# Kernel tuning notes

Measured on AMD Instinct MI355X. Metric: run time of the kernel, lower is better.

## Reference

```python
import jax, jax.numpy as jnp
import numpy as np

B, N, D, H = 2, 2048, 1024, 16
HD = D // H
SCALE = HD ** -0.5


def setup_inputs() -> dict:
    key = jax.random.key(0)
    ks = jax.random.split(key, 9)
    s = D ** -0.5
    return {
        "x": jax.random.normal(ks[0], (B, N, D), dtype=jnp.float32),
        "Wq": jax.random.normal(ks[1], (D, D), dtype=jnp.float32) * s,
        "bq": jax.random.normal(ks[2], (D,), dtype=jnp.float32) * 0.01,
        "Wk": jax.random.normal(ks[3], (D, D), dtype=jnp.float32) * s,
        "bk": jax.random.normal(ks[4], (D,), dtype=jnp.float32) * 0.01,
        "Wv": jax.random.normal(ks[5], (D, D), dtype=jnp.float32) * s,
        "bv": jax.random.normal(ks[6], (D,), dtype=jnp.float32) * 0.01,
        "Wo": jax.random.normal(ks[7], (D, D), dtype=jnp.float32) * s,
        "bo": jax.random.normal(ks[8], (D,), dtype=jnp.float32) * 0.01,
    }


def reference(x, Wq, bq, Wk, bk, Wv, bv, Wo, bo):
    # Q/K/V projections (torch Linear: x @ W.T + b), split into heads: (B,H,N,HD)
    def proj(W, b):
        return (x @ W.T + b).reshape(B, N, H, HD).transpose(0, 2, 1, 3)

    q = proj(Wq, bq)
    k = proj(Wk, bk)
    v = proj(Wv, bv)
    # Scaled dot-product attention with explicit (B,H,N,N) scores
    scores = jnp.einsum("bhnd,bhmd->bhnm", q, k) * SCALE
    attn = jax.nn.softmax(scores, axis=-1)
    y = jnp.einsum("bhnm,bhmd->bhnd", attn, v)
    y = y.transpose(0, 2, 1, 3).reshape(B, N, D)
    # Output projection
    return y @ Wo.T + bo
```

## Files before the change

kernel.cpp:

```cpp
#include <hip/hip_runtime.h>

#define BB 2
#define NN 2048
#define DD 1024
#define HH 16
#define HD 64
#define SCALE 0.125f

typedef unsigned short u16;
typedef unsigned int u32;
typedef __attribute__((ext_vector_type(2))) unsigned int u32x2;
typedef __attribute__((ext_vector_type(4))) short short4v;
typedef __attribute__((ext_vector_type(8))) short short8;
typedef __attribute__((ext_vector_type(4))) float float4v;
typedef __attribute__((ext_vector_type(16))) float f32x16;

__device__ __forceinline__ float b2f(u16 u) {
    union { float f; u32 i; } x; x.i = ((u32)u) << 16; return x.f;
}
__device__ __forceinline__ u16 f2b(float f) {
    union { float f; u32 i; } x; x.f = f;
    u32 i = x.i;
    return (u16)((i + 0x7fffu + ((i >> 16) & 1u)) >> 16);
}

#if __has_builtin(__builtin_amdgcn_exp2f)
#define EXP2F(x) __builtin_amdgcn_exp2f(x)
#else
#define EXP2F(x) __expf((x) * 0.69314718055994531f)
#endif

#if __has_builtin(__builtin_amdgcn_rcpf)
#define RCPF(x) __builtin_amdgcn_rcpf(x)
#else
#define RCPF(x) (1.0f / (x))
#endif

#if __has_builtin(__builtin_amdgcn_permlane32_swap)
#define PSWAP(a, b, ra, rb)                                                  \
    { u32x2 _r = __builtin_amdgcn_permlane32_swap((a), (b), false, false);   \
      (ra) = _r[0]; (rb) = _r[1]; }
#else
#define PSWAP(a, b, ra, rb)                                                  \
    { u32 _xa = (u32)__shfl_xor((int)(a), 32, 64);                           \
      u32 _xb = (u32)__shfl_xor((int)(b), 32, 64);                           \
      (ra) = hi ? _xb : (a); (rb) = hi ? (b) : _xa; }
#endif

__device__ __forceinline__ u32 cvtpk(float a, float b) {
    u32 r;
    asm("v_cvt_pk_bf16_f32 %0, %1, %2" : "=v"(r) : "v"(a), "v"(b));
    return r;
}

__device__ __forceinline__ void gl_lds16(const u16* g, u16* l) {
    __builtin_amdgcn_global_load_lds(
        (__attribute__((address_space(1))) void*)(void*)g,
        (__attribute__((address_space(3))) void*)l, 16, 0, 0);
}

__global__ __launch_bounds__(256) void cvt_all(
    const float* __restrict__ x,
    const float* __restrict__ Wq, const float* __restrict__ Wk,
    const float* __restrict__ Wv, const float* __restrict__ Wo,
    u16* __restrict__ xb, u16* __restrict__ W4)
{
    int e = (blockIdx.x * 256 + threadIdx.x) * 8;
    const float* s;
    u16* d;
    if (e < 4194304) { s = x + e; d = xb + e; }
    else {
        int e2 = e - 4194304;
        int which = e2 >> 20;
        int off = e2 & 1048575;
        s = ((which == 0) ? Wq : (which == 1) ? Wk : (which == 2) ? Wv : Wo) + off;
        d = W4 + e2;
    }
    float4v a = *(const float4v*)s;
    float4v b = *(const float4v*)(s + 4);
    short8 r;
    r[0] = (short)f2b(a[0]); r[1] = (short)f2b(a[1]);
    r[2] = (short)f2b(a[2]); r[3] = (short)f2b(a[3]);
    r[4] = (short)f2b(b[0]); r[5] = (short)f2b(b[1]);
    r[6] = (short)f2b(b[2]); r[7] = (short)f2b(b[3]);
    *(short8*)d = r;
}

__global__ __launch_bounds__(512) void gemm_qkv(
    const u16* __restrict__ xb,
    const u16* __restrict__ Wqb, const float* __restrict__ bq,
    const u16* __restrict__ Wkb, const float* __restrict__ bk,
    const u16* __restrict__ Wvb, const float* __restrict__ bv,
    u16* __restrict__ Qo, u16* __restrict__ Ko, u16* __restrict__ Vt)
{
    const int lid = blockIdx.y * 12 + blockIdx.x;
    const int seq = (lid & 7) * 24 + (lid >> 3);
    const int tm = seq / 12;
    const int tn = seq % 12;
    const int mat = tn >> 2;
    const int tnq = tn & 3;

    const u16* __restrict__ W     = (mat == 0) ? Wqb : (mat == 1) ? Wkb : Wvb;
    const float* __restrict__ bias = (mat == 0) ? bq : (mat == 1) ? bk : bv;

    __shared__ u16 As[4][256 * 32];
    __shared__ u16 Bs[4][256 * 32];

    const int tid  = threadIdx.x;
    const int wave = tid >> 6, lane = tid & 63;
    const int wm = wave >> 2, wn = wave & 3;
    const int quad = lane >> 4, l16 = lane & 15;

    const int sr = tid >> 2, sc = tid & 3;
    const u16* ga0 = &xb[(size_t)(tm * 256 + sr) * DD + sc * 8];
    const u16* ga1 = ga0 + (size_t)128 * DD;
    const u16* gb0 = &W [(size_t)(tnq * 256 + sr) * DD + sc * 8];
    const u16* gb1 = gb0 + (size_t)128 * DD;

    float4v acc[8][4] = {};

    #pragma unroll
    for (int s = 0; s < 3; ++s) {
        const int ks = s << 5;
        gl_lds16(ga0 + ks, &As[s][tid * 8]);
        gl_lds16(ga1 + ks, &As[s][(512 + tid) * 8]);
        gl_lds16(gb0 + ks, &Bs[s][tid * 8]);
        gl_lds16(gb1 + ks, &Bs[s][(512 + tid) * 8]);
    }

    for (int it = 0; it < 32; ++it) {
        asm volatile("s_waitcnt vmcnt(8)" ::: "memory");
        __builtin_amdgcn_s_barrier();

        const int k3 = ((it + 3) & 31) << 5;
        const int b3 = (it + 3) & 3;
        gl_lds16(ga0 + k3, &As[b3][tid * 8]);
        gl_lds16(ga1 + k3, &As[b3][(512 + tid) * 8]);
        gl_lds16(gb0 + k3, &Bs[b3][tid * 8]);
        gl_lds16(gb1 + k3, &Bs[b3][(512 + tid) * 8]);

        const int cb = it & 3;
        short8 af[8], bf[4];
        #pragma unroll
        for (int mi = 0; mi < 8; ++mi)
            af[mi] = *(const short8*)&As[cb][(wm * 128 + mi * 16 + l16) * 32 + quad * 8];
        #pragma unroll
        for (int ni = 0; ni < 4; ++ni)
            bf[ni] = *(const short8*)&Bs[cb][(wn * 64 + ni * 16 + l16) * 32 + quad * 8];

        #pragma unroll
        for (int mi = 0; mi < 8; ++mi)
            #pragma unroll
            for (int ni = 0; ni < 4; ++ni)
                acc[mi][ni] = __builtin_amdgcn_mfma_f32_16x16x32_bf16(
                    af[mi], bf[ni], acc[mi][ni], 0, 0, 0);
    }
    asm volatile("s_waitcnt vmcnt(0)" ::: "memory");

    #pragma unroll
    for (int mi = 0; mi < 8; ++mi) {
        #pragma unroll
        for (int ni = 0; ni < 4; ++ni) {
            int cc = tnq * 256 + wn * 64 + ni * 16 + l16;
            int h = cc >> 6, hd = cc & 63;
            float bv_ = bias[cc];
            if (mat == 2) {
                short4v v4;
                #pragma unroll
                for (int rr = 0; rr < 4; ++rr)
                    v4[rr] = (short)f2b(acc[mi][ni][rr] + bv_);
                int R0 = tm * 256 + wm * 128 + mi * 16 + quad * 4;
                int b = R0 >> 11, n = R0 & 2047;
                *(short4v*)&Vt[(((size_t)(b * HH + h)) * HD + hd) * NN + n] = v4;
            } else {
                u16* Out = (mat == 0) ? Qo : Ko;
                #pragma unroll
                for (int rr = 0; rr < 4; ++rr) {
                    int R = tm * 256 + wm * 128 + mi * 16 + quad * 4 + rr;
                    int b = R >> 11, n = R & 2047;
                    Out[(((size_t)(b * HH + h)) * NN + n) * HD + hd] =
                        f2b(acc[mi][ni][rr] + bv_);
                }
            }
        }
    }
}

__global__ __launch_bounds__(256) void gemm_out(
    const u16* __restrict__ A, const u16* __restrict__ W,
    const float* __restrict__ bias, float* __restrict__ Out)
{
    const int tm = blockIdx.y;
    const int tn = blockIdx.x;

    __shared__ u16 As[4][64 * 32];
    __shared__ u16 Bs[4][128 * 32];

    const int tid  = threadIdx.x;
    const int wave = tid >> 6, lane = tid & 63;
    const int quad = lane >> 4, l16 = lane & 15;
    const int wn = wave;

    const int r0 = tid >> 2, c0 = tid & 3;

    const u16* ga  = &A[(size_t)(tm * 64 + r0) * DD + c0 * 8];
    const u16* gb0 = &W[(size_t)(tn * 128 + r0) * DD + c0 * 8];
    const u16* gb1 = &W[(size_t)(tn * 128 + r0 + 64) * DD + c0 * 8];

    float4v acc[4][2] = {};

    #pragma unroll
    for (int s = 0; s < 3; ++s) {
        const int ks = s << 5;
        gl_lds16(ga + ks,  &As[s][tid * 8]);
        gl_lds16(gb0 + ks, &Bs[s][tid * 8]);
        gl_lds16(gb1 + ks, &Bs[s][(256 + tid) * 8]);
    }

    for (int it = 0; it < 32; ++it) {
        asm volatile("s_waitcnt vmcnt(6)" ::: "memory");
        __builtin_amdgcn_s_barrier();

        const int k3 = ((it + 3) & 31) << 5;
        const int b3 = (it + 3) & 3;
        gl_lds16(ga + k3,  &As[b3][tid * 8]);
        gl_lds16(gb0 + k3, &Bs[b3][tid * 8]);
        gl_lds16(gb1 + k3, &Bs[b3][(256 + tid) * 8]);

        const int cb = it & 3;
        short8 af[4], bf[2];
        #pragma unroll
        for (int mi = 0; mi < 4; ++mi)
            af[mi] = *(const short8*)&As[cb][(mi * 16 + l16) * 32 + quad * 8];
        #pragma unroll
        for (int ni = 0; ni < 2; ++ni)
            bf[ni] = *(const short8*)&Bs[cb][(wn * 32 + ni * 16 + l16) * 32 + quad * 8];

        #pragma unroll
        for (int mi = 0; mi < 4; ++mi)
            #pragma unroll
            for (int ni = 0; ni < 2; ++ni)
                acc[mi][ni] = __builtin_amdgcn_mfma_f32_16x16x32_bf16(
                    af[mi], bf[ni], acc[mi][ni], 0, 0, 0);
    }
    asm volatile("s_waitcnt vmcnt(0)" ::: "memory");

    #pragma unroll
    for (int mi = 0; mi < 4; ++mi) {
        #pragma unroll
        for (int ni = 0; ni < 2; ++ni) {
            int cc = tn * 128 + wn * 32 + ni * 16 + l16;
            float bv_ = bias[cc];
            #pragma unroll
            for (int rr = 0; rr < 4; ++rr) {
                int R = tm * 64 + mi * 16 + quad * 4 + rr;
                Out[(size_t)R * DD + cc] = acc[mi][ni][rr] + bv_;
            }
        }
    }
}

__global__ __launch_bounds__(256) void attn_mfma(
    const u16* __restrict__ Q, const u16* __restrict__ K,
    const u16* __restrict__ Vt, u16* __restrict__ Y)
{
    const int id   = blockIdx.x;
    const int xcd  = id & 7;
    const int slot = id >> 3;
    const int bh   = (xcd << 2) | (slot & 3);
    const int qb   = slot >> 2;

    const int tid  = threadIdx.x;
    const int wave = tid >> 6, lane = tid & 63;
    const int l31  = lane & 31, hi = lane >> 5;

    const u16* __restrict__ Qb = Q + (size_t)bh * NN * HD;
    const u16* __restrict__ Kb = K + (size_t)bh * NN * HD;
    const u16* __restrict__ Vb = Vt + (size_t)bh * HD * NN;

    __shared__ u16 Ks[2][64 * 64];
    __shared__ u16 Vs[2][64 * 64];

    short8 qf[4];
    {
        int qrow = qb * 128 + wave * 32 + l31;
        #pragma unroll
        for (int c = 0; c < 4; ++c) {
            short8 t = *(const short8*)&Qb[(size_t)qrow * HD + c * 16 + hi * 8];
            #pragma unroll
            for (int j = 0; j < 8; ++j)
                qf[c][j] = (short)f2b(b2f((u16)t[j]) * SCALE);
        }
    }

    short8 onesB;
    #pragma unroll
    for (int j = 0; j < 8; ++j) onesB[j] = (short)0x3F80;

    f32x16 oc[2] = {};
    f32x16 la = {};

    const int srow = tid >> 3, sslot = tid & 7;
    const int oA = (sslot + srow) & 7;
    const int oB = (sslot + srow + 32) & 7;

    gl_lds16(&Kb[(size_t)srow * HD + oA * 8],          &Ks[0][tid * 8]);
    gl_lds16(&Kb[(size_t)(srow + 32) * HD + oB * 8],   &Ks[0][(256 + tid) * 8]);
    gl_lds16(&Vb[(size_t)srow * NN + oA * 8],          &Vs[0][tid * 8]);
    gl_lds16(&Vb[(size_t)(srow + 32) * NN + oB * 8],   &Vs[0][(256 + tid) * 8]);

    for (int k0 = 0; k0 < NN; k0 += 64) {
        const int cur = (k0 >> 6) & 1;
        const int kn = (k0 + 64) & (NN - 1);

        __syncthreads();

        gl_lds16(&Kb[(size_t)(kn + srow) * HD + oA * 8],      &Ks[cur ^ 1][tid * 8]);
        gl_lds16(&Kb[(size_t)(kn + srow + 32) * HD + oB * 8], &Ks[cur ^ 1][(256 + tid) * 8]);
        gl_lds16(&Vb[(size_t)srow * NN + kn + oA * 8],        &Vs[cur ^ 1][tid * 8]);
        gl_lds16(&Vb[(size_t)(srow + 32) * NN + kn + oB * 8], &Vs[cur ^ 1][(256 + tid) * 8]);

        f32x16 st[2];
        __builtin_amdgcn_s_setprio(1);
        #pragma unroll
        for (int kt = 0; kt < 2; ++kt) {
            f32x16 z = {};
            const int row = kt * 32 + l31;
            #pragma unroll
            for (int c = 0; c < 4; ++c) {
                short8 kf = *(const short8*)
                    &Ks[cur][row * 64 + ((2 * c + hi - row) & 7) * 8];
                z = __builtin_amdgcn_mfma_f32_32x32x16_bf16(kf, qf[c], z, 0, 0, 0);
            }
            st[kt] = z;
        }
        __builtin_amdgcn_s_setprio(0);

        u32 pk0[8], pk1[8];
        #pragma unroll
        for (int i = 0; i < 8; ++i) {
            float a0 = EXP2F(__builtin_fmaf(st[0][2 * i],     1.44269504f, -11.5415603f));
            float a1 = EXP2F(__builtin_fmaf(st[0][2 * i + 1], 1.44269504f, -11.5415603f));
            pk0[i] = cvtpk(a0, a1);
            float b0 = EXP2F(__builtin_fmaf(st[1][2 * i],     1.44269504f, -11.5415603f));
            float b1 = EXP2F(__builtin_fmaf(st[1][2 * i + 1], 1.44269504f, -11.5415603f));
            pk1[i] = cvtpk(b0, b1);
        }

        short8 pa[4];
        {
            union { u32 w[4]; short8 s; } lo, hi_;
            PSWAP(pk0[0], pk0[2], lo.w[0], lo.w[2]);
            PSWAP(pk0[1], pk0[3], lo.w[1], lo.w[3]);
            PSWAP(pk0[4], pk0[6], hi_.w[0], hi_.w[2]);
            PSWAP(pk0[5], pk0[7], hi_.w[1], hi_.w[3]);
            pa[0] = lo.s; pa[1] = hi_.s;
            PSWAP(pk1[0], pk1[2], lo.w[0], lo.w[2]);
            PSWAP(pk1[1], pk1[3], lo.w[1], lo.w[3]);
            PSWAP(pk1[4], pk1[6], hi_.w[0], hi_.w[2]);
            PSWAP(pk1[5], pk1[7], hi_.w[1], hi_.w[3]);
            pa[2] = lo.s; pa[3] = hi_.s;
        }

        __builtin_amdgcn_s_setprio(1);
        #pragma unroll
        for (int ks = 0; ks < 4; ++ks)
            la = __builtin_amdgcn_mfma_f32_32x32x16_bf16(pa[ks], onesB, la, 0, 0, 0);
        #pragma unroll
        for (int ks = 0; ks < 4; ++ks) {
            #pragma unroll
            for (int ht = 0; ht < 2; ++ht) {
                const int row = ht * 32 + l31;
                short8 vf = *(const short8*)
                    &Vs[cur][row * 64 + ((2 * ks + hi - row) & 7) * 8];
                oc[ht] = __builtin_amdgcn_mfma_f32_32x32x16_bf16(pa[ks], vf, oc[ht], 0, 0, 0);
            }
        }
        __builtin_amdgcn_s_setprio(0);
    }
    asm volatile("s_waitcnt vmcnt(0)" ::: "memory");

    const int b = bh >> 4, h = bh & 15;
    #pragma unroll
    for (int r = 0; r < 16; ++r) {
        const int n = qb * 128 + wave * 32 + (r & 3) + 8 * (r >> 2) + 4 * hi;
        const float iv = RCPF(la[r]);
        #pragma unroll
        for (int ht = 0; ht < 2; ++ht) {
            const int col = h * HD + ht * 32 + l31;
            Y[((size_t)(b * NN + n)) * DD + col] = f2b(oc[ht][r] * iv);
        }
    }
}

extern "C" void kernel_launch(void* const* d_in, const int* in_sizes, int n_in,
                              void* d_out, int out_size, void* d_ws, size_t ws_size,
                              hipStream_t stream) {
    const float* x  = (const float*)d_in[0];
    const float* Wq = (const float*)d_in[1];
    const float* bq = (const float*)d_in[2];
    const float* Wk = (const float*)d_in[3];
    const float* bk = (const float*)d_in[4];
    const float* Wv = (const float*)d_in[5];
    const float* bv = (const float*)d_in[6];
    const float* Wo = (const float*)d_in[7];
    const float* bo = (const float*)d_in[8];
    float* out = (float*)d_out;

    const size_t M1 = 1024 * 1024;
    u16* base = (u16*)d_ws;
    u16* xb  = base;
    u16* W4  = base + 4 * M1;
    u16* Wqb = W4;
    u16* Wkb = W4 + 1 * M1;
    u16* Wvb = W4 + 2 * M1;
    u16* Wob = W4 + 3 * M1;
    u16* Qw  = base + 8 * M1;
    u16* Kw  = base + 12 * M1;
    u16* Vtw = base + 16 * M1;
    u16* Yw  = xb;

    cvt_all<<<dim3(4096), 256, 0, stream>>>(x, Wq, Wk, Wv, Wo, xb, W4);

    gemm_qkv<<<dim3(12, 16), 512, 0, stream>>>(xb, Wqb, bq, Wkb, bk, Wvb, bv,
                                               Qw, Kw, Vtw);

    attn_mfma<<<dim3(512), 256, 0, stream>>>(Qw, Kw, Vtw, Yw);

    gemm_out<<<dim3(8, 64), 256, 0, stream>>>(Yw, Wob, bo, out);
}
```

Baseline: 206.7 us.

## Double block sizes in attention and output GEMM with deeper LDS pipelining

The attention kernel now uses 512-thread blocks covering 256 query rows, so each K/V tile staged in LDS serves twice as many queries. It also moves from double to four-deep buffering with a counted vmcnt wait and raw barrier instead of __syncthreads. The output GEMM grows to 128x128 tiles with 8 waves, halving A/W tile reloads per output. Grid sizes drop to 256 attention blocks and 256 GEMM blocks, which may lower occupancy and wave-level parallelism on a 256-CU device.

```diff
diff --git a/kernel.cpp b/kernel.cpp
--- a/kernel.cpp
+++ b/kernel.cpp
@@ -186,52 +186,48 @@
     }
 }
 
-__global__ __launch_bounds__(256) void gemm_out(
+__global__ __launch_bounds__(512) void gemm_out(
     const u16* __restrict__ A, const u16* __restrict__ W,
     const float* __restrict__ bias, float* __restrict__ Out)
 {
+    const int tn = blockIdx.x;
     const int tm = blockIdx.y;
-    const int tn = blockIdx.x;
-
-    __shared__ u16 As[4][64 * 32];
+
+    __shared__ u16 As[4][128 * 32];
     __shared__ u16 Bs[4][128 * 32];
 
     const int tid  = threadIdx.x;
     const int wave = tid >> 6, lane = tid & 63;
+    const int wm = wave >> 2, wn = wave & 3;
     const int quad = lane >> 4, l16 = lane & 15;
-    const int wn = wave;
-
-    const int r0 = tid >> 2, c0 = tid & 3;
-
-    const u16* ga  = &A[(size_t)(tm * 64 + r0) * DD + c0 * 8];
-    const u16* gb0 = &W[(size_t)(tn * 128 + r0) * DD + c0 * 8];
-    const u16* gb1 = &W[(size_t)(tn * 128 + r0 + 64) * DD + c0 * 8];
+
+    const int sr = tid >> 2, sc = tid & 3;
+    const u16* ga = &A[(size_t)(tm * 128 + sr) * DD + sc * 8];
+    const u16* gb = &W[(size_t)(tn * 128 + sr) * DD + sc * 8];
 
     float4v acc[4][2] = {};
 
     #pragma unroll
     for (int s = 0; s < 3; ++s) {
         const int ks = s << 5;
-        gl_lds16(ga + ks,  &As[s][tid * 8]);
-        gl_lds16(gb0 + ks, &Bs[s][tid * 8]);
-        gl_lds16(gb1 + ks, &Bs[s][(256 + tid) * 8]);
+        gl_lds16(ga + ks, &As[s][tid * 8]);
+        gl_lds16(gb + ks, &Bs[s][tid * 8]);
     }
 
     for (int it = 0; it < 32; ++it) {
-        asm volatile("s_waitcnt vmcnt(6)" ::: "memory");
+        asm volatile("s_waitcnt vmcnt(4)" ::: "memory");
         __builtin_amdgcn_s_barrier();
 
         const int k3 = ((it + 3) & 31) << 5;
         const int b3 = (it + 3) & 3;
-        gl_lds16(ga + k3,  &As[b3][tid * 8]);
-        gl_lds16(gb0 + k3, &Bs[b3][tid * 8]);
-        gl_lds16(gb1 + k3, &Bs[b3][(256 + tid) * 8]);
+        gl_lds16(ga + k3, &As[b3][tid * 8]);
+        gl_lds16(gb + k3, &Bs[b3][tid * 8]);
 
         const int cb = it & 3;
         short8 af[4], bf[2];
         #pragma unroll
         for (int mi = 0; mi < 4; ++mi)
-            af[mi] = *(const short8*)&As[cb][(mi * 16 + l16) * 32 + quad * 8];
+            af[mi] = *(const short8*)&As[cb][(wm * 64 + mi * 16 + l16) * 32 + quad * 8];
         #pragma unroll
         for (int ni = 0; ni < 2; ++ni)
             bf[ni] = *(const short8*)&Bs[cb][(wn * 32 + ni * 16 + l16) * 32 + quad * 8];
@@ -253,14 +249,14 @@
             float bv_ = bias[cc];
             #pragma unroll
             for (int rr = 0; rr < 4; ++rr) {
-                int R = tm * 64 + mi * 16 + quad * 4 + rr;
+                int R = tm * 128 + wm * 64 + mi * 16 + quad * 4 + rr;
                 Out[(size_t)R * DD + cc] = acc[mi][ni][rr] + bv_;
             }
         }
     }
 }
 
-__global__ __launch_bounds__(256) void attn_mfma(
+__global__ __launch_bounds__(512) void attn_mfma(
     const u16* __restrict__ Q, const u16* __restrict__ K,
     const u16* __restrict__ Vt, u16* __restrict__ Y)
 {
@@ -278,12 +274,12 @@
     const u16* __restrict__ Kb = K + (size_t)bh * NN * HD;
     const u16* __restrict__ Vb = Vt + (size_t)bh * HD * NN;
 
-    __shared__ u16 Ks[2][64 * 64];
-    __shared__ u16 Vs[2][64 * 64];
+    __shared__ u16 Ks[4][64 * 64];
+    __shared__ u16 Vs[4][64 * 64];
 
     short8 qf[4];
     {
-        int qrow = qb * 128 + wave * 32 + l31;
+        int qrow = qb * 256 + wave * 32 + l31;
         #pragma unroll
         for (int c = 0; c < 4; ++c) {
             short8 t = *(const short8*)&Qb[(size_t)qrow * HD + c * 16 + hi * 8];
@@ -301,24 +297,25 @@
     f32x16 la = {};
 
     const int srow = tid >> 3, sslot = tid & 7;
-    const int oA = (sslot + srow) & 7;
-    const int oB = (sslot + srow + 32) & 7;
-
-    gl_lds16(&Kb[(size_t)srow * HD + oA * 8],          &Ks[0][tid * 8]);
-    gl_lds16(&Kb[(size_t)(srow + 32) * HD + oB * 8],   &Ks[0][(256 + tid) * 8]);
-    gl_lds16(&Vb[(size_t)srow * NN + oA * 8],          &Vs[0][tid * 8]);
-    gl_lds16(&Vb[(size_t)(srow + 32) * NN + oB * 8],   &Vs[0][(256 + tid) * 8]);
-
-    for (int k0 = 0; k0 < NN; k0 += 64) {
-        const int cur = (k0 >> 6) & 1;
-        const int kn = (k0 + 64) & (NN - 1);
-
-        __syncthreads();
-
-        gl_lds16(&Kb[(size_t)(kn + srow) * HD + oA * 8],      &Ks[cur ^ 1][tid * 8]);
-        gl_lds16(&Kb[(size_t)(kn + srow + 32) * HD + oB * 8], &Ks[cur ^ 1][(256 + tid) * 8]);
-        gl_lds16(&Vb[(size_t)srow * NN + kn + oA * 8],        &Vs[cur ^ 1][tid * 8]);
-        gl_lds16(&Vb[(size_t)(srow + 32) * NN + kn + oB * 8], &Vs[cur ^ 1][(256 + tid) * 8]);
+    const int oct = (sslot + srow) & 7;
+
+    #pragma unroll
+    for (int s = 0; s < 3; ++s) {
+        const int ks = s * 64;
+        gl_lds16(&Kb[(size_t)(ks + srow) * HD + oct * 8], &Ks[s][tid * 8]);
+        gl_lds16(&Vb[(size_t)srow * NN + ks + oct * 8],   &Vs[s][tid * 8]);
+    }
+
+    for (int it = 0; it < 32; ++it) {
+        asm volatile("s_waitcnt vmcnt(4)" ::: "memory");
+        __builtin_amdgcn_s_barrier();
+
+        const int k3 = ((it + 3) & 31) * 64;
+        const int b3 = (it + 3) & 3;
+        gl_lds16(&Kb[(size_t)(k3 + srow) * HD + oct * 8], &Ks[b3][tid * 8]);
+        gl_lds16(&Vb[(size_t)srow * NN + k3 + oct * 8],   &Vs[b3][tid * 8]);
+
+        const int cur = it & 3;
 
         f32x16 st[2];
         __builtin_amdgcn_s_setprio(1);
@@ -383,7 +380,7 @@
     const int b = bh >> 4, h = bh & 15;
     #pragma unroll
     for (int r = 0; r < 16; ++r) {
-        const int n = qb * 128 + wave * 32 + (r & 3) + 8 * (r >> 2) + 4 * hi;
+        const int n = qb * 256 + wave * 32 + (r & 3) + 8 * (r >> 2) + 4 * hi;
         const float iv = RCPF(la[r]);
         #pragma unroll
         for (int ht = 0; ht < 2; ++ht) {
@@ -425,7 +422,7 @@
     gemm_qkv<<<dim3(12, 16), 512, 0, stream>>>(xb, Wqb, bq, Wkb, bk, Wvb, bv,
                                                Qw, Kw, Vtw);
 
-    attn_mfma<<<dim3(512), 256, 0, stream>>>(Qw, Kw, Vtw, Yw);
-
-    gemm_out<<<dim3(8, 64), 256, 0, stream>>>(Yw, Wob, bo, out);
-}
+    attn_mfma<<<dim3(256), 512, 0, stream>>>(Qw, Kw, Vtw, Yw);
+
+    gemm_out<<<dim3(8, 32), 512, 0, stream>>>(Yw, Wob, bo, out);
+}
```

Measured after the change: 203.4 us. About the same (-1.6%).
